# Kernel tuning notes

Measured on AMD Instinct MI355X. Metric: run time of the kernel, lower is better.

The kernel has to match this reference:

```python
import jax, jax.numpy as jnp
import numpy as np

IN_D = 512
VOCAB = 32000
SEQ = 2048

def setup_inputs() -> dict:
    key = jax.random.key(0)
    ks = jax.random.split(key, 12)
    d = IN_D
    def xavier(k, shape):
        fan_in, fan_out = shape[1], shape[0]
        a = jnp.sqrt(6.0 / (fan_in + fan_out))
        return jax.random.uniform(k, shape, jnp.float32, -a, a)
    return {
        'X': jax.random.randint(ks[0], (1, SEQ), 0, VOCAB),
        'wz': xavier(ks[1], (VOCAB, d)),
        'uz': xavier(ks[2], (d, d)),
        'w': xavier(ks[3], (VOCAB, d)),
        'u': xavier(ks[4], (d, d)),
        'wr': xavier(ks[5], (VOCAB, d)),
        'ur': xavier(ks[6], (d, d)),
        'wy': xavier(ks[7], (VOCAB, d)),
        'bz': xavier(ks[8], (1, d)),
        'br': xavier(ks[9], (1, d)),
        'bh': xavier(ks[10], (1, d)),
        'by': xavier(ks[11], (1, VOCAB)),
    }

def reference(X, wz, uz, w, u, wr, ur, wy, bz, br, bh, by):
    idx = X[0]                      # (T,) batch is hardcoded to 1 in original
    ez = wz[idx]                    # (T, d) per-step embedding gathers, done once
    er = wr[idx]
    eh = w[idx]

    def step(h, emb):
        e_z, e_r, e_h = emb
        z = jax.nn.sigmoid(e_z + h @ uz.T + bz[0])
        r = jax.nn.sigmoid(e_r + h @ ur.T + br[0])
        h_xh = jnp.tanh(e_h + (r * h) @ u.T + bh[0])
        h_new = h * z + (1.0 - z) * h_xh
        return h_new, h_new

    h0 = jnp.zeros((wz.shape[1],), dtype=wz.dtype)
    _, hs = jax.lax.scan(step, h0, (ez, er, eh))   # hs: (T, d)
    logits = hs @ wy.T + by[0]                     # (T, vocab)
    outs = jax.nn.log_softmax(logits, axis=-1)     # matches squeeze(0)
    hiddens = hs[None, :, :]                       # (1, T, d)
    return outs, hiddens
```

## Files before the change

kernel.cpp:

```cpp
#include <hip/hip_runtime.h>
#include <math.h>

typedef unsigned short u16;
typedef unsigned short us8 __attribute__((ext_vector_type(8)));
typedef short bf16x8 __attribute__((ext_vector_type(8)));
typedef float f32x4 __attribute__((ext_vector_type(4)));

#define D       512
#define SEQ     2048
#define VOCAB   32000
#define NB      16
#define RPB     32
#define STPB    512
#define FSTRIDE 16

__device__ __forceinline__ u16 f2bf(float f) {
    union { float f; unsigned i; } x; x.f = f;
    unsigned r = x.i + 0x7fff + ((x.i >> 16) & 1);
    return (u16)(r >> 16);
}

__device__ __forceinline__ float agent_ld(const float* p) {
    return __hip_atomic_load(p, __ATOMIC_RELAXED, __HIP_MEMORY_SCOPE_AGENT);
}
__device__ __forceinline__ void agent_st(float* p, float v) {
    __hip_atomic_store(p, v, __ATOMIC_RELAXED, __HIP_MEMORY_SCOPE_AGENT);
}
__device__ __forceinline__ int flag_ld(const int* p) {
    return __hip_atomic_load(p, __ATOMIC_RELAXED, __HIP_MEMORY_SCOPE_AGENT);
}
__device__ __forceinline__ void flag_st(int* p, int v) {
    __hip_atomic_store(p, v, __ATOMIC_RELAXED, __HIP_MEMORY_SCOPE_AGENT);
}

__global__ void init_scratch(int* __restrict__ flags, float* __restrict__ hbuf,
                             float* __restrict__ rhbuf)
{
    const int t = threadIdx.x;
    if (t < NB * FSTRIDE) flags[t] = 0;
    hbuf[t]  = 0.f;
    rhbuf[t] = 0.f;
}

__global__ __launch_bounds__(STPB, 2) void scan_kernel(
    const int* __restrict__ X,
    const float* __restrict__ WZ, const float* __restrict__ UZ,
    const float* __restrict__ W,  const float* __restrict__ U,
    const float* __restrict__ WR, const float* __restrict__ UR,
    const float* __restrict__ BZ, const float* __restrict__ BR,
    const float* __restrict__ BH,
    int* __restrict__ flags, float* __restrict__ hbuf, float* __restrict__ rhbuf,
    float* __restrict__ outH)
{
    __shared__ int   idxsm[SEQ];
    __shared__ float hsm[(D / 32) * 33];

    const int tid = threadIdx.x, b = blockIdx.x;
    const int r  = tid >> 4;
    const int cg = tid & 15;
    const int c0 = cg * 32;
    const int g  = b * RPB + r;

    for (int i = tid; i < SEQ; i += STPB) idxsm[i] = X[i];

    float uzw[32], urw[32], uw[32];
#pragma unroll
    for (int j = 0; j < 32; j += 4) {
        f32x4 vz = *(const f32x4*)&UZ[(size_t)g * D + c0 + j];
        f32x4 vr = *(const f32x4*)&UR[(size_t)g * D + c0 + j];
        f32x4 vu = *(const f32x4*)&U [(size_t)g * D + c0 + j];
#pragma unroll
        for (int q = 0; q < 4; ++q) {
            uzw[j + q] = vz[q];
            urw[j + q] = vr[q];
            uw [j + q] = vu[q];
        }
    }
    const float bzv = BZ[g], brv = BR[g], bhv = BH[g];
    __syncthreads();

    const int i0 = idxsm[0];
    float ezc = WZ[(size_t)i0 * D + g];
    float erc = WR[(size_t)i0 * D + g];
    float ehc = W [(size_t)i0 * D + g];

#pragma unroll 1
    for (int t = 0; t < SEQ; ++t) {
        const int tn = (t + 1 < SEQ) ? t + 1 : t;
        const int in_ = idxsm[tn];
        const float pz = WZ[(size_t)in_ * D + g];
        const float pr = WR[(size_t)in_ * D + g];
        const float ph = W [(size_t)in_ * D + g];

        if (tid < 128) {
            const int e = tid * 4;
            float v0 = agent_ld(&hbuf[e + 0]);
            float v1 = agent_ld(&hbuf[e + 1]);
            float v2 = agent_ld(&hbuf[e + 2]);
            float v3 = agent_ld(&hbuf[e + 3]);
            float* p = &hsm[(e >> 5) * 33 + (e & 31)];
            p[0] = v0; p[1] = v1; p[2] = v2; p[3] = v3;
        }
        __syncthreads();

        float az = 0.f, ar = 0.f;
#pragma unroll
        for (int j = 0; j < 32; ++j) {
            float hj = hsm[cg * 33 + j];
            az = fmaf(uzw[j], hj, az);
            ar = fmaf(urw[j], hj, ar);
        }
#pragma unroll
        for (int mk = 8; mk; mk >>= 1) {
            az += __shfl_xor(az, mk);
            ar += __shfl_xor(ar, mk);
        }
        const float hrow = hsm[b * 33 + r];
        const float zz = 1.f / (1.f + __expf(-(ezc + az + bzv)));
        const float rr = 1.f / (1.f + __expf(-(erc + ar + brv)));
        if (cg == 0) agent_st(&rhbuf[g], rr * hrow);
        __syncthreads();
        if (tid == 0) flag_st(&flags[b * FSTRIDE], 2 * t + 1);
        if (tid < NB) { while (flag_ld(&flags[tid * FSTRIDE]) < 2 * t + 1) {} }
        __syncthreads();

        if (tid < 128) {
            const int e = tid * 4;
            float v0 = agent_ld(&rhbuf[e + 0]);
            float v1 = agent_ld(&rhbuf[e + 1]);
            float v2 = agent_ld(&rhbuf[e + 2]);
            float v3 = agent_ld(&rhbuf[e + 3]);
            float* p = &hsm[(e >> 5) * 33 + (e & 31)];
            p[0] = v0; p[1] = v1; p[2] = v2; p[3] = v3;
        }
        __syncthreads();

        float ah = 0.f;
#pragma unroll
        for (int j = 0; j < 32; ++j) {
            float xj = hsm[cg * 33 + j];
            ah = fmaf(uw[j], xj, ah);
        }
#pragma unroll
        for (int mk = 8; mk; mk >>= 1) ah += __shfl_xor(ah, mk);

        const float hxh  = tanhf(ehc + ah + bhv);
        const float hnew = hrow * zz + (1.f - zz) * hxh;
        if (cg == 0) {
            agent_st(&hbuf[g], hnew);
            outH[(size_t)t * D + g] = hnew;
        }
        __syncthreads();
        if (tid == 0) flag_st(&flags[b * FSTRIDE], 2 * t + 2);
        if (tid < NB) { while (flag_ld(&flags[tid * FSTRIDE]) < 2 * t + 2) {} }
        __syncthreads();

        ezc = pz; erc = pr; ehc = ph;
    }
}

#define GBM 128
#define GBN 128
#define GBK 64

__global__ __launch_bounds__(256) void gemm_logits(
    const float* __restrict__ A,
    const float* __restrict__ B,
    const float* __restrict__ BY,
    float* __restrict__ C)
{
    __shared__ __align__(16) u16 As[GBM * GBK];
    __shared__ __align__(16) u16 Bs[GBN * GBK];

    const int tid = threadIdx.x;
    const int wv = tid >> 6, lane = tid & 63;
    const int lr = lane & 15, lg = lane >> 4;
    const int bm = blockIdx.y, bn = blockIdx.x;
    const int wm = (wv >> 1) * 64, wn = (wv & 1) * 64;

    const int srow = tid >> 3;
    const int scol = (tid & 7) * 8;

    f32x4 acc[4][4] = {};

    for (int kt = 0; kt < D; kt += GBK) {
        __syncthreads();
#pragma unroll
        for (int p = 0; p < 4; ++p) {
            const int row = p * 32 + srow;
            f32x4 a0 = *(const f32x4*)&A[(size_t)(bm * GBM + row) * D + kt + scol];
            f32x4 a1 = *(const f32x4*)&A[(size_t)(bm * GBM + row) * D + kt + scol + 4];
            f32x4 b0 = *(const f32x4*)&B[(size_t)(bn * GBN + row) * D + kt + scol];
            f32x4 b1 = *(const f32x4*)&B[(size_t)(bn * GBN + row) * D + kt + scol + 4];
            us8 oa, ob;
#pragma unroll
            for (int q = 0; q < 4; ++q) {
                oa[q] = f2bf(a0[q]); oa[4 + q] = f2bf(a1[q]);
                ob[q] = f2bf(b0[q]); ob[4 + q] = f2bf(b1[q]);
            }
            *(us8*)&As[row * GBK + scol] = oa;
            *(us8*)&Bs[row * GBK + scol] = ob;
        }
        __syncthreads();
#pragma unroll
        for (int kk = 0; kk < 2; ++kk) {
            bf16x8 af[4], bfr[4];
#pragma unroll
            for (int mi = 0; mi < 4; ++mi)
                af[mi] = *(const bf16x8*)&As[(wm + mi * 16 + lr) * GBK + kk * 32 + lg * 8];
#pragma unroll
            for (int ni = 0; ni < 4; ++ni)
                bfr[ni] = *(const bf16x8*)&Bs[(wn + ni * 16 + lr) * GBK + kk * 32 + lg * 8];
#pragma unroll
            for (int mi = 0; mi < 4; ++mi)
#pragma unroll
                for (int ni = 0; ni < 4; ++ni)
                    acc[mi][ni] = __builtin_amdgcn_mfma_f32_16x16x32_bf16(
                        af[mi], bfr[ni], acc[mi][ni], 0, 0, 0);
        }
    }

#pragma unroll
    for (int ni = 0; ni < 4; ++ni) {
        const int n = bn * GBN + wn + ni * 16 + lr;
        const float byv = BY[n];
#pragma unroll
        for (int mi = 0; mi < 4; ++mi) {
#pragma unroll
            for (int q = 0; q < 4; ++q) {
                const int m = bm * GBM + wm + mi * 16 + lg * 4 + q;
                C[(size_t)m * VOCAB + n] = acc[mi][ni][q] + byv;
            }
        }
    }
}

__global__ __launch_bounds__(256) void logsoftmax_kernel(float* __restrict__ C)
{
    const int m = blockIdx.x;
    float* row = C + (size_t)m * VOCAB;
    const int tid = threadIdx.x;

    float s = 0.f;
    for (int v = tid; v < VOCAB / 4; v += 256) {
        f32x4 x = *(const f32x4*)&row[v * 4];
        s += __expf(x[0]) + __expf(x[1]) + __expf(x[2]) + __expf(x[3]);
    }
#pragma unroll
    for (int mk = 32; mk; mk >>= 1) s += __shfl_xor(s, mk);
    __shared__ float red[4];
    if ((tid & 63) == 0) red[tid >> 6] = s;
    __syncthreads();
    const float lse = __logf(red[0] + red[1] + red[2] + red[3]);

    for (int v = tid; v < VOCAB / 4; v += 256) {
        f32x4 x = *(const f32x4*)&row[v * 4];
        x[0] -= lse; x[1] -= lse; x[2] -= lse; x[3] -= lse;
        *(f32x4*)&row[v * 4] = x;
    }
}

extern "C" void kernel_launch(void* const* d_in, const int* in_sizes, int n_in,
                              void* d_out, int out_size, void* d_ws, size_t ws_size,
                              hipStream_t stream)
{
    const int*   X  = (const int*)d_in[0];
    const float* wz = (const float*)d_in[1];
    const float* uz = (const float*)d_in[2];
    const float* w  = (const float*)d_in[3];
    const float* u  = (const float*)d_in[4];
    const float* wr = (const float*)d_in[5];
    const float* ur = (const float*)d_in[6];
    const float* wy = (const float*)d_in[7];
    const float* bz = (const float*)d_in[8];
    const float* br = (const float*)d_in[9];
    const float* bh = (const float*)d_in[10];
    const float* by = (const float*)d_in[11];

    float* out  = (float*)d_out;
    float* outH = out + (size_t)SEQ * VOCAB;

    char* scratch = (ws_size >= 8192) ? (char*)d_ws : (char*)d_out;
    int*   flags = (int*)scratch;
    float* hbuf  = (float*)(scratch + 1024);
    float* rhbuf = (float*)(scratch + 3072);

    init_scratch<<<1, STPB, 0, stream>>>(flags, hbuf, rhbuf);

    scan_kernel<<<NB, STPB, 0, stream>>>(X, wz, uz, w, u, wr, ur, bz, br, bh,
                                         flags, hbuf, rhbuf, outH);

    dim3 ggrid(VOCAB / GBN, SEQ / GBM);
    gemm_logits<<<ggrid, 256, 0, stream>>>(outH, wy, by, out);

    logsoftmax_kernel<<<SEQ, 256, 0, stream>>>(out);
}
```

Baseline: 8.350 ms.

## Replace flag barriers with step-tagged 64-bit values in scan exchange

The scan kernel's cross-block grid barriers, which used per-block flags and spins, are replaced by packing each hidden or r*h value with its timestep tag into a 64-bit word. Readers spin until every needed element carries the current tag. This removes two flag store/spin round trips and one __syncthreads per half-step, so blocks synchronize only on the data they consume. The cost is doubled exchange-buffer traffic and a reliance on 64-bit atomic stores being single-copy atomic. Tag comparisons must also stay correct when a fast block overwrites a value with a newer step.

```diff
diff --git a/kernel.cpp b/kernel.cpp
--- a/kernel.cpp
+++ b/kernel.cpp
@@ -2,6 +2,7 @@
 #include <math.h>
 
 typedef unsigned short u16;
+typedef unsigned long long u64;
 typedef unsigned short us8 __attribute__((ext_vector_type(8)));
 typedef short bf16x8 __attribute__((ext_vector_type(8)));
 typedef float f32x4 __attribute__((ext_vector_type(4)));
@@ -12,7 +13,6 @@
 #define NB      16
 #define RPB     32
 #define STPB    512
-#define FSTRIDE 16
 
 __device__ __forceinline__ u16 f2bf(float f) {
     union { float f; unsigned i; } x; x.f = f;
@@ -20,26 +20,26 @@
     return (u16)(r >> 16);
 }
 
-__device__ __forceinline__ float agent_ld(const float* p) {
+__device__ __forceinline__ u64 tag_ld(const u64* p) {
     return __hip_atomic_load(p, __ATOMIC_RELAXED, __HIP_MEMORY_SCOPE_AGENT);
 }
-__device__ __forceinline__ void agent_st(float* p, float v) {
+__device__ __forceinline__ void tag_st(u64* p, u64 v) {
     __hip_atomic_store(p, v, __ATOMIC_RELAXED, __HIP_MEMORY_SCOPE_AGENT);
 }
-__device__ __forceinline__ int flag_ld(const int* p) {
-    return __hip_atomic_load(p, __ATOMIC_RELAXED, __HIP_MEMORY_SCOPE_AGENT);
-}
-__device__ __forceinline__ void flag_st(int* p, int v) {
-    __hip_atomic_store(p, v, __ATOMIC_RELAXED, __HIP_MEMORY_SCOPE_AGENT);
-}
-
-__global__ void init_scratch(int* __restrict__ flags, float* __restrict__ hbuf,
-                             float* __restrict__ rhbuf)
+__device__ __forceinline__ u64 packtv(float f, unsigned tag) {
+    union { float f; unsigned i; } x; x.f = f;
+    return ((u64)tag << 32) | (u64)x.i;
+}
+__device__ __forceinline__ float unpackv(u64 v) {
+    union { unsigned i; float f; } x; x.i = (unsigned)v;
+    return x.f;
+}
+
+__global__ void init_scratch(u64* __restrict__ hbuf, u64* __restrict__ rhbuf)
 {
     const int t = threadIdx.x;
-    if (t < NB * FSTRIDE) flags[t] = 0;
-    hbuf[t]  = 0.f;
-    rhbuf[t] = 0.f;
+    hbuf[t]  = 0ull;
+    rhbuf[t] = 0ull;
 }
 
 __global__ __launch_bounds__(STPB, 2) void scan_kernel(
@@ -49,7 +49,7 @@
     const float* __restrict__ WR, const float* __restrict__ UR,
     const float* __restrict__ BZ, const float* __restrict__ BR,
     const float* __restrict__ BH,
-    int* __restrict__ flags, float* __restrict__ hbuf, float* __restrict__ rhbuf,
+    u64* __restrict__ hbuf, u64* __restrict__ rhbuf,
     float* __restrict__ outH)
 {
     __shared__ int   idxsm[SEQ];
@@ -91,15 +91,24 @@
         const float pz = WZ[(size_t)in_ * D + g];
         const float pr = WR[(size_t)in_ * D + g];
         const float ph = W [(size_t)in_ * D + g];
+        const unsigned ta = (unsigned)t;
+        const unsigned tb = (unsigned)t + 1u;
 
         if (tid < 128) {
             const int e = tid * 4;
-            float v0 = agent_ld(&hbuf[e + 0]);
-            float v1 = agent_ld(&hbuf[e + 1]);
-            float v2 = agent_ld(&hbuf[e + 2]);
-            float v3 = agent_ld(&hbuf[e + 3]);
+            u64 v0, v1, v2, v3;
+            for (;;) {
+                v0 = tag_ld(&hbuf[e + 0]);
+                v1 = tag_ld(&hbuf[e + 1]);
+                v2 = tag_ld(&hbuf[e + 2]);
+                v3 = tag_ld(&hbuf[e + 3]);
+                if ((unsigned)(v0 >> 32) >= ta && (unsigned)(v1 >> 32) >= ta &&
+                    (unsigned)(v2 >> 32) >= ta && (unsigned)(v3 >> 32) >= ta)
+                    break;
+            }
             float* p = &hsm[(e >> 5) * 33 + (e & 31)];
-            p[0] = v0; p[1] = v1; p[2] = v2; p[3] = v3;
+            p[0] = unpackv(v0); p[1] = unpackv(v1);
+            p[2] = unpackv(v2); p[3] = unpackv(v3);
         }
         __syncthreads();
 
@@ -118,20 +127,24 @@
         const float hrow = hsm[b * 33 + r];
         const float zz = 1.f / (1.f + __expf(-(ezc + az + bzv)));
         const float rr = 1.f / (1.f + __expf(-(erc + ar + brv)));
-        if (cg == 0) agent_st(&rhbuf[g], rr * hrow);
-        __syncthreads();
-        if (tid == 0) flag_st(&flags[b * FSTRIDE], 2 * t + 1);
-        if (tid < NB) { while (flag_ld(&flags[tid * FSTRIDE]) < 2 * t + 1) {} }
+        if (cg == 0) tag_st(&rhbuf[g], packtv(rr * hrow, tb));
         __syncthreads();
 
         if (tid < 128) {
             const int e = tid * 4;
-            float v0 = agent_ld(&rhbuf[e + 0]);
-            float v1 = agent_ld(&rhbuf[e + 1]);
-            float v2 = agent_ld(&rhbuf[e + 2]);
-            float v3 = agent_ld(&rhbuf[e + 3]);
+            u64 v0, v1, v2, v3;
+            for (;;) {
+                v0 = tag_ld(&rhbuf[e + 0]);
+                v1 = tag_ld(&rhbuf[e + 1]);
+                v2 = tag_ld(&rhbuf[e + 2]);
+                v3 = tag_ld(&rhbuf[e + 3]);
+                if ((unsigned)(v0 >> 32) >= tb && (unsigned)(v1 >> 32) >= tb &&
+                    (unsigned)(v2 >> 32) >= tb && (unsigned)(v3 >> 32) >= tb)
+                    break;
+            }
             float* p = &hsm[(e >> 5) * 33 + (e & 31)];
-            p[0] = v0; p[1] = v1; p[2] = v2; p[3] = v3;
+            p[0] = unpackv(v0); p[1] = unpackv(v1);
+            p[2] = unpackv(v2); p[3] = unpackv(v3);
         }
         __syncthreads();
 
@@ -147,12 +160,9 @@
         const float hxh  = tanhf(ehc + ah + bhv);
         const float hnew = hrow * zz + (1.f - zz) * hxh;
         if (cg == 0) {
-            agent_st(&hbuf[g], hnew);
+            tag_st(&hbuf[g], packtv(hnew, tb));
             outH[(size_t)t * D + g] = hnew;
         }
-        __syncthreads();
-        if (tid == 0) flag_st(&flags[b * FSTRIDE], 2 * t + 2);
-        if (tid < NB) { while (flag_ld(&flags[tid * FSTRIDE]) < 2 * t + 2) {} }
         __syncthreads();
 
         ezc = pz; erc = pr; ehc = ph;
@@ -281,14 +291,13 @@
     float* outH = out + (size_t)SEQ * VOCAB;
 
     char* scratch = (ws_size >= 8192) ? (char*)d_ws : (char*)d_out;
-    int*   flags = (int*)scratch;
-    float* hbuf  = (float*)(scratch + 1024);
-    float* rhbuf = (float*)(scratch + 3072);
-
-    init_scratch<<<1, STPB, 0, stream>>>(flags, hbuf, rhbuf);
+    u64* hbuf  = (u64*)scratch;
+    u64* rhbuf = (u64*)(scratch + 4096);
+
+    init_scratch<<<1, STPB, 0, stream>>>(hbuf, rhbuf);
 
     scan_kernel<<<NB, STPB, 0, stream>>>(X, wz, uz, w, u, wr, ur, bz, br, bh,
-                                         flags, hbuf, rhbuf, outH);
+                                         hbuf, rhbuf, outH);
 
     dim3 ggrid(VOCAB / GBN, SEQ / GBM);
     gemm_logits<<<ggrid, 256, 0, stream>>>(outH, wy, by, out);
```

Measured after the change: 6.843 ms. 1.22x faster.
